# Kernel optimization log

Hardware: AMD Instinct MI355X
Metric: run time of the kernel (lower is better)

## Reference

```python
import math
import jax, jax.numpy as jnp
import numpy as np

MODEL_DIM = 4096
NUM_EXPERTS = 64
NUM_TOKENS = 8192
CAPACITY_FACTOR = 1.0


def setup_inputs() -> dict:
    key = jax.random.key(0)
    kx, kw = jax.random.split(key)
    x = jax.random.normal(kx, (NUM_TOKENS, MODEL_DIM), dtype=jnp.float32)
    # nn.Linear weight: [num_experts, model_dim]
    W = jax.random.normal(kw, (NUM_EXPERTS, MODEL_DIM), dtype=jnp.float32) * (1.0 / math.sqrt(MODEL_DIM))
    return {"x": x, "W": W}


def reference(x, W):
    # gating projection (no bias), cast to fp32 as in top1gating
    logits = jnp.matmul(x, W.T).astype(jnp.float32)  # [S, E]
    num_tokens, num_experts = logits.shape
    capacity = int(CAPACITY_FACTOR * math.ceil(num_tokens / num_experts))

    indices1_s = jnp.argmax(logits, axis=1)                        # [S]
    gates = jax.nn.softmax(logits, axis=1)                         # [S, E]
    mask1 = jax.nn.one_hot(indices1_s, num_experts, dtype=jnp.float32)  # [S, E]
    gates1_s = jnp.sum(gates * mask1, axis=1)                      # [S]
    # per-expert running position of each routed token
    locations1 = jnp.cumsum(mask1, axis=0) - 1.0                   # [S, E]
    locations1_s = jnp.sum(locations1 * mask1, axis=1)             # [S]

    return (indices1_s.astype(jnp.int32),
            capacity,
            locations1_s.astype(jnp.int32),
            gates1_s,
            num_experts)
```

## Files before the change

### kernel.cpp

```cpp
#include <hip/hip_runtime.h>
#include <math.h>

#define NTOK 8192
#define MDIM 4096
#define NEXP 64
#define CAPACITY 128.0f

#define OFF_IDX  0
#define OFF_CAP  8192
#define OFF_LOC  8193
#define OFF_GATE 16385
#define OFF_NE   24577

#define KC 64

#define WS_CNT_OFF  0
#define WS_RK_OFF   8192
#define WS_W_OFF    16384
#define WS_PART_OFF (16384 + (3 * NEXP * MDIM) / 2)

using bf16x8 = __attribute__((ext_vector_type(8))) short;
using f32x4  = __attribute__((ext_vector_type(4))) float;

static __device__ __forceinline__ unsigned short f2bf(float f) {
    union { float f; unsigned u; } v; v.f = f;
    unsigned r = v.u + 0x7fffu + ((v.u >> 16) & 1u);
    return (unsigned short)(r >> 16);
}
static __device__ __forceinline__ float bf2f(unsigned short h) {
    union { unsigned u; float f; } v; v.u = ((unsigned)h) << 16;
    return v.f;
}

__global__ __launch_bounds__(256) void prep_w(
    const float* __restrict__ W, unsigned short* __restrict__ Ws)
{
    const int gid = blockIdx.x * 256 + threadIdx.x;
    const int e   = gid >> 10;
    const int f4  = gid & 1023;
    float4 v = ((const float4*)W)[e * 1024 + f4];
    float av[4] = {v.x, v.y, v.z, v.w};
    unsigned short h[3][4];
    #pragma unroll
    for (int j = 0; j < 4; ++j) {
        float a = av[j];
        unsigned short b1 = f2bf(a);  float r1 = a  - bf2f(b1);
        unsigned short b2 = f2bf(r1); float r2 = r1 - bf2f(b2);
        unsigned short b3 = f2bf(r2);
        h[0][j] = b1; h[1][j] = b2; h[2][j] = b3;
    }
    #pragma unroll
    for (int t = 0; t < 3; ++t)
        *(ushort4*)&Ws[((size_t)(t * 64 + e)) * MDIM + f4 * 4] =
            make_ushort4(h[t][0], h[t][1], h[t][2], h[t][3]);
}

template<int S>
__global__ __launch_bounds__(256, 3) void gate_mfma(
    const float* __restrict__ x,
    const unsigned short* __restrict__ Ws,
    float* __restrict__ part)
{
    constexpr int KSL = MDIM / S;
    constexpr int NCH = KSL / KC;

    __shared__ __align__(16) float4 xs[2][4][16][16];

    const int tid   = threadIdx.x;
    const int lane  = tid & 63;
    const int wv    = tid >> 6;
    const int m     = lane & 15;
    const int g     = lane >> 4;
    const int tok0  = blockIdx.x * 64;
    const int slice = blockIdx.y;
    const int k0    = slice * KSL;

    const float4* __restrict__ x4 = (const float4*)x;
    const unsigned short* __restrict__ wp =
        Ws + (size_t)m * MDIM + k0 + g * 8;

    auto stage = [&](int c, int b) {
        #pragma unroll
        for (int j = 0; j < 4; ++j) {
            const int tl  = j * 4 + (lane >> 4);
            const int src = (lane & 15) ^ (tl & 7);
            const float4* gsrc = x4 + (size_t)(tok0 + wv * 16 + tl) * (MDIM / 4)
                                 + (k0 >> 2) + c * 16 + src;
            void* ldst = (void*)&xs[b][wv][j * 4][0];
            __builtin_amdgcn_global_load_lds(
                (const __attribute__((address_space(1))) void*)gsrc,
                (__attribute__((address_space(3))) void*)ldst, 16, 0, 0);
        }
    };

    auto readx = [&](int b, int ks, float4& lo, float4& hi) {
        const int l0 = ks * 8 + g * 2;
        lo = xs[b][wv][m][(l0    ) ^ (m & 7)];
        hi = xs[b][wv][m][(l0 + 1) ^ (m & 7)];
    };

    auto cvt = [&](float4 lo, float4 hi, bf16x8& r0, bf16x8& r1, bf16x8& r2) {
        float f[8] = {lo.x, lo.y, lo.z, lo.w, hi.x, hi.y, hi.z, hi.w};
        #pragma unroll
        for (int j = 0; j < 8; ++j) {
            float a = f[j];
            unsigned short b1 = f2bf(a);  float t1 = a  - bf2f(b1);
            unsigned short b2 = f2bf(t1); float t2 = t1 - bf2f(b2);
            unsigned short b3 = f2bf(t2);
            r0[j] = (short)b1; r1[j] = (short)b2; r2[j] = (short)b3;
        }
    };

    f32x4 acc[4];
    #pragma unroll
    for (int nt = 0; nt < 4; ++nt) acc[nt] = (f32x4){0.f, 0.f, 0.f, 0.f};

    auto step = [&](const bf16x8* a, bf16x8 w[3][4]) {
        #pragma unroll
        for (int nt = 0; nt < 4; ++nt)
            acc[nt] = __builtin_amdgcn_mfma_f32_16x16x32_bf16(a[2], w[0][nt], acc[nt], 0, 0, 0);
        #pragma unroll
        for (int nt = 0; nt < 4; ++nt)
            acc[nt] = __builtin_amdgcn_mfma_f32_16x16x32_bf16(a[0], w[2][nt], acc[nt], 0, 0, 0);
        #pragma unroll
        for (int nt = 0; nt < 4; ++nt)
            acc[nt] = __builtin_amdgcn_mfma_f32_16x16x32_bf16(a[1], w[1][nt], acc[nt], 0, 0, 0);
        #pragma unroll
        for (int nt = 0; nt < 4; ++nt)
            acc[nt] = __builtin_amdgcn_mfma_f32_16x16x32_bf16(a[1], w[0][nt], acc[nt], 0, 0, 0);
        #pragma unroll
        for (int nt = 0; nt < 4; ++nt)
            acc[nt] = __builtin_amdgcn_mfma_f32_16x16x32_bf16(a[0], w[1][nt], acc[nt], 0, 0, 0);
        #pragma unroll
        for (int nt = 0; nt < 4; ++nt)
            acc[nt] = __builtin_amdgcn_mfma_f32_16x16x32_bf16(a[0], w[0][nt], acc[nt], 0, 0, 0);
    };

    stage(0, 0);

    for (int c = 0; c < NCH; ++c) {
        const int cur = c & 1;
        if (c + 1 < NCH) stage(c + 1, cur ^ 1);

        bf16x8 w0[3][4], w1[3][4];
        const unsigned short* q = wp + c * KC;
        #pragma unroll
        for (int t = 0; t < 3; ++t)
            #pragma unroll
            for (int nt = 0; nt < 4; ++nt)
                w0[t][nt] = *(const bf16x8*)(q + (size_t)(t * 64 + nt * 16) * MDIM);

        float4 lo0, hi0, lo1, hi1;
        readx(cur, 0, lo0, hi0);
        readx(cur, 1, lo1, hi1);
        bf16x8 a0[3], a1[3];
        cvt(lo0, hi0, a0[0], a0[1], a0[2]);
        cvt(lo1, hi1, a1[0], a1[1], a1[2]);

        #pragma unroll
        for (int t = 0; t < 3; ++t)
            #pragma unroll
            for (int nt = 0; nt < 4; ++nt)
                w1[t][nt] = *(const bf16x8*)(q + (size_t)(t * 64 + nt * 16) * MDIM + 32);

        step(a0, w0);
        step(a1, w1);
    }

    #pragma unroll
    for (int nt = 0; nt < 4; ++nt)
        #pragma unroll
        for (int r = 0; r < 4; ++r) {
            const int tokr = tok0 + wv * 16 + g * 4 + r;
            part[((size_t)slice * NTOK + tokr) * 64 + nt * 16 + m] = acc[nt][r];
        }
}

template<int S>
__global__ __launch_bounds__(256) void reduce_count(
    const float* __restrict__ part,
    float* __restrict__ out,
    int* __restrict__ cnt,
    int* __restrict__ rk)
{
    __shared__ int eidx[64];

    const int tid  = threadIdx.x;
    const int lane = tid & 63;
    const int wv   = tid >> 6;
    const int tok0 = blockIdx.x * 64;
    const int trel = wv * 16 + (lane >> 2);
    const int tok  = tok0 + trel;
    const int q    = lane & 3;

    const float4* __restrict__ p4 = (const float4*)part;

    float4 a[4];
    #pragma unroll
    for (int r = 0; r < 4; ++r) a[r] = make_float4(0.f, 0.f, 0.f, 0.f);
    for (int s = 0; s < S; ++s) {
        #pragma unroll
        for (int r = 0; r < 4; ++r) {
            float4 v = p4[((size_t)s * NTOK + tok) * 16 + q * 4 + r];
            a[r].x += v.x; a[r].y += v.y; a[r].z += v.z; a[r].w += v.w;
        }
    }

    float vals[16];
    #pragma unroll
    for (int r = 0; r < 4; ++r) {
        vals[r * 4 + 0] = a[r].x; vals[r * 4 + 1] = a[r].y;
        vals[r * 4 + 2] = a[r].z; vals[r * 4 + 3] = a[r].w;
    }

    float bm = vals[0];
    int   be = q * 16;
    #pragma unroll
    for (int j = 1; j < 16; ++j)
        if (vals[j] > bm) { bm = vals[j]; be = q * 16 + j; }
    #pragma unroll
    for (int off = 1; off <= 2; off <<= 1) {
        float om = __shfl_xor(bm, off, 64);
        int   oe = __shfl_xor(be, off, 64);
        if (om > bm || (om == bm && oe < be)) { bm = om; be = oe; }
    }

    float es = 0.f;
    #pragma unroll
    for (int j = 0; j < 16; ++j) es += expf(vals[j] - bm);
    #pragma unroll
    for (int off = 1; off <= 2; off <<= 1)
        es += __shfl_xor(es, off, 64);

    if (q == 0) {
        out[OFF_IDX  + tok] = (float)be;
        out[OFF_GATE + tok] = 1.0f / es;
        eidx[trel] = be;
    }
    __syncthreads();

    if (tid < 64) {
        const int e = eidx[tid];
        const unsigned long long lt =
            (tid == 0) ? 0ull : ((~0ull) >> (64 - tid));
        unsigned long long mymask = 0;
        int myrk = 0;
        for (int ee = 0; ee < 64; ++ee) {
            unsigned long long mb = __ballot(e == ee);
            if (tid == ee) mymask = mb;
            if (e == ee)   myrk   = (int)__popcll(mb & lt);
        }
        cnt[blockIdx.x * 64 + tid] = (int)__popcll(mymask);
        rk[tok0 + tid] = myrk;
    }
    if (tid == 0 && blockIdx.x == 0) {
        out[OFF_CAP] = CAPACITY;
        out[OFF_NE]  = (float)NEXP;
    }
}

__global__ __launch_bounds__(1024) void scan_final(
    const float* __restrict__ idxf,
    const int* __restrict__ cnt,
    const int* __restrict__ rk,
    float* __restrict__ out)
{
    __shared__ int lcnt[128 * 64];
    __shared__ int wtot[16 * 64];

    const int tid  = threadIdx.x;
    const int lane = tid & 63;
    const int w    = tid >> 6;

    #pragma unroll
    for (int j = 0; j < 8; ++j) lcnt[j * 1024 + tid] = cnt[j * 1024 + tid];
    __syncthreads();

    {
        int sum = 0;
        #pragma unroll
        for (int j = 0; j < 8; ++j) sum += lcnt[(w * 8 + j) * 64 + lane];
        wtot[w * 64 + lane] = sum;
    }
    __syncthreads();

    if (tid < 64) {
        int run = 0;
        #pragma unroll
        for (int w2 = 0; w2 < 16; ++w2) {
            int t = wtot[w2 * 64 + tid];
            wtot[w2 * 64 + tid] = run;
            run += t;
        }
    }
    __syncthreads();

    {
        int run = wtot[w * 64 + lane];
        #pragma unroll
        for (int j = 0; j < 8; ++j) {
            int c = w * 8 + j;
            int v = lcnt[c * 64 + lane];
            lcnt[c * 64 + lane] = run;
            run += v;
        }
    }
    __syncthreads();

    #pragma unroll
    for (int j = 0; j < 8; ++j) {
        int s = j * 1024 + tid;
        int e = (int)idxf[s];
        out[OFF_LOC + s] = (float)(lcnt[(s >> 6) * 64 + e] + rk[s]);
    }
}

extern "C" void kernel_launch(void* const* d_in, const int* in_sizes, int n_in,
                              void* d_out, int out_size, void* d_ws, size_t ws_size,
                              hipStream_t stream)
{
    const float* x = (const float*)d_in[0];
    const float* W = (const float*)d_in[1];
    float* out = (float*)d_out;

    int*   cnt  = (int*)d_ws + WS_CNT_OFF;
    int*   rk   = (int*)d_ws + WS_RK_OFF;
    unsigned short* Ws = (unsigned short*)((int*)d_ws + WS_W_OFF);
    float* part = (float*)d_ws + WS_PART_OFF;

    prep_w<<<256, 256, 0, stream>>>(W, Ws);

    const size_t base = (size_t)WS_PART_OFF * 4;
    const size_t per_slice = (size_t)NTOK * 64 * 4;

    if (ws_size >= base + 8 * per_slice) {
        gate_mfma<8><<<dim3(128, 8), 256, 0, stream>>>(x, Ws, part);
        reduce_count<8><<<128, 256, 0, stream>>>(part, out, cnt, rk);
    } else if (ws_size >= base + 4 * per_slice) {
        gate_mfma<4><<<dim3(128, 4), 256, 0, stream>>>(x, Ws, part);
        reduce_count<4><<<128, 256, 0, stream>>>(part, out, cnt, rk);
    } else if (ws_size >= base + 2 * per_slice) {
        gate_mfma<2><<<dim3(128, 2), 256, 0, stream>>>(x, Ws, part);
        reduce_count<2><<<128, 256, 0, stream>>>(part, out, cnt, rk);
    } else {
        gate_mfma<1><<<dim3(128, 1), 256, 0, stream>>>(x, Ws, part);
        reduce_count<1><<<128, 256, 0, stream>>>(part, out, cnt, rk);
    }

    scan_final<<<1, 1024, 0, stream>>>(out + OFF_IDX, cnt, rk, out);
}
```

Baseline: 273.4 us.

## Retile gating GEMM to single-wave 32-token blocks and parallelize location scan

The gating matmul now uses one-wave blocks covering 32 tokens (two 16-row groups sharing each weight fragment) with a 32-wide K chunk, and splits K into up to 16 slices, so the grid has many more blocks. The reduce kernel is adapted to 32-token blocks. The single-block 1024-thread scan is replaced by a per-expert wave-shuffle scan kernel plus a parallel emit kernel. The aim is better CU occupancy and latency hiding, and removing the serial single-block tail. In exchange there are more partial-sum writes and reads and an extra kernel launch.

```diff
diff --git a/kernel.cpp b/kernel.cpp
--- a/kernel.cpp
+++ b/kernel.cpp
@@ -12,12 +12,15 @@
 #define OFF_GATE 16385
 #define OFF_NE   24577
 
-#define KC 64
+#define KC 32
+
+#define NCHK 256
 
 #define WS_CNT_OFF  0
-#define WS_RK_OFF   8192
-#define WS_W_OFF    16384
-#define WS_PART_OFF (16384 + (3 * NEXP * MDIM) / 2)
+#define WS_RK_OFF   16384
+#define WS_SB_OFF   24576
+#define WS_W_OFF    40960
+#define WS_PART_OFF (40960 + (3 * NEXP * MDIM) / 2)
 
 using bf16x8 = __attribute__((ext_vector_type(8))) short;
 using f32x4  = __attribute__((ext_vector_type(4))) float;
@@ -56,7 +59,7 @@
 }
 
 template<int S>
-__global__ __launch_bounds__(256, 3) void gate_mfma(
+__global__ __launch_bounds__(64, 3) void gate_mfma(
     const float* __restrict__ x,
     const unsigned short* __restrict__ Ws,
     float* __restrict__ part)
@@ -64,14 +67,12 @@
     constexpr int KSL = MDIM / S;
     constexpr int NCH = KSL / KC;
 
-    __shared__ __align__(16) float4 xs[2][4][16][16];
-
-    const int tid   = threadIdx.x;
-    const int lane  = tid & 63;
-    const int wv    = tid >> 6;
+    __shared__ __align__(16) float4 xs[2][32][8];
+
+    const int lane  = threadIdx.x & 63;
     const int m     = lane & 15;
     const int g     = lane >> 4;
-    const int tok0  = blockIdx.x * 64;
+    const int tok0  = blockIdx.x * 32;
     const int slice = blockIdx.y;
     const int k0    = slice * KSL;
 
@@ -82,21 +83,15 @@
     auto stage = [&](int c, int b) {
         #pragma unroll
         for (int j = 0; j < 4; ++j) {
-            const int tl  = j * 4 + (lane >> 4);
-            const int src = (lane & 15) ^ (tl & 7);
-            const float4* gsrc = x4 + (size_t)(tok0 + wv * 16 + tl) * (MDIM / 4)
-                                 + (k0 >> 2) + c * 16 + src;
-            void* ldst = (void*)&xs[b][wv][j * 4][0];
+            const int row  = j * 8 + (lane >> 3);
+            const int srcs = (lane & 7) ^ (row & 7);
+            const float4* gsrc = x4 + (size_t)(tok0 + row) * (MDIM / 4)
+                                 + (k0 >> 2) + c * 8 + srcs;
+            void* ldst = (void*)&xs[b][j * 8][0];
             __builtin_amdgcn_global_load_lds(
                 (const __attribute__((address_space(1))) void*)gsrc,
                 (__attribute__((address_space(3))) void*)ldst, 16, 0, 0);
         }
-    };
-
-    auto readx = [&](int b, int ks, float4& lo, float4& hi) {
-        const int l0 = ks * 8 + g * 2;
-        lo = xs[b][wv][m][(l0    ) ^ (m & 7)];
-        hi = xs[b][wv][m][(l0 + 1) ^ (m & 7)];
     };
 
     auto cvt = [&](float4 lo, float4 hi, bf16x8& r0, bf16x8& r1, bf16x8& r2) {
@@ -111,69 +106,77 @@
         }
     };
 
-    f32x4 acc[4];
-    #pragma unroll
-    for (int nt = 0; nt < 4; ++nt) acc[nt] = (f32x4){0.f, 0.f, 0.f, 0.f};
-
-    auto step = [&](const bf16x8* a, bf16x8 w[3][4]) {
-        #pragma unroll
-        for (int nt = 0; nt < 4; ++nt)
-            acc[nt] = __builtin_amdgcn_mfma_f32_16x16x32_bf16(a[2], w[0][nt], acc[nt], 0, 0, 0);
-        #pragma unroll
-        for (int nt = 0; nt < 4; ++nt)
-            acc[nt] = __builtin_amdgcn_mfma_f32_16x16x32_bf16(a[0], w[2][nt], acc[nt], 0, 0, 0);
-        #pragma unroll
-        for (int nt = 0; nt < 4; ++nt)
-            acc[nt] = __builtin_amdgcn_mfma_f32_16x16x32_bf16(a[1], w[1][nt], acc[nt], 0, 0, 0);
-        #pragma unroll
-        for (int nt = 0; nt < 4; ++nt)
-            acc[nt] = __builtin_amdgcn_mfma_f32_16x16x32_bf16(a[1], w[0][nt], acc[nt], 0, 0, 0);
-        #pragma unroll
-        for (int nt = 0; nt < 4; ++nt)
-            acc[nt] = __builtin_amdgcn_mfma_f32_16x16x32_bf16(a[0], w[1][nt], acc[nt], 0, 0, 0);
-        #pragma unroll
-        for (int nt = 0; nt < 4; ++nt)
-            acc[nt] = __builtin_amdgcn_mfma_f32_16x16x32_bf16(a[0], w[0][nt], acc[nt], 0, 0, 0);
-    };
+    f32x4 acc[2][4];
+    #pragma unroll
+    for (int gr = 0; gr < 2; ++gr)
+        #pragma unroll
+        for (int nt = 0; nt < 4; ++nt) acc[gr][nt] = (f32x4){0.f, 0.f, 0.f, 0.f};
 
     stage(0, 0);
 
     for (int c = 0; c < NCH; ++c) {
         const int cur = c & 1;
+
+        bf16x8 w[3][4];
+        const unsigned short* q = wp + c * KC;
+        #pragma unroll
+        for (int t = 0; t < 3; ++t)
+            #pragma unroll
+            for (int nt = 0; nt < 4; ++nt)
+                w[t][nt] = *(const bf16x8*)(q + (size_t)(t * 64 + nt * 16) * MDIM);
+
         if (c + 1 < NCH) stage(c + 1, cur ^ 1);
 
-        bf16x8 w0[3][4], w1[3][4];
-        const unsigned short* q = wp + c * KC;
-        #pragma unroll
-        for (int t = 0; t < 3; ++t)
-            #pragma unroll
-            for (int nt = 0; nt < 4; ++nt)
-                w0[t][nt] = *(const bf16x8*)(q + (size_t)(t * 64 + nt * 16) * MDIM);
-
-        float4 lo0, hi0, lo1, hi1;
-        readx(cur, 0, lo0, hi0);
-        readx(cur, 1, lo1, hi1);
-        bf16x8 a0[3], a1[3];
-        cvt(lo0, hi0, a0[0], a0[1], a0[2]);
-        cvt(lo1, hi1, a1[0], a1[1], a1[2]);
-
-        #pragma unroll
-        for (int t = 0; t < 3; ++t)
-            #pragma unroll
-            for (int nt = 0; nt < 4; ++nt)
-                w1[t][nt] = *(const bf16x8*)(q + (size_t)(t * 64 + nt * 16) * MDIM + 32);
-
-        step(a0, w0);
-        step(a1, w1);
-    }
-
-    #pragma unroll
-    for (int nt = 0; nt < 4; ++nt)
-        #pragma unroll
-        for (int r = 0; r < 4; ++r) {
-            const int tokr = tok0 + wv * 16 + g * 4 + r;
-            part[((size_t)slice * NTOK + tokr) * 64 + nt * 16 + m] = acc[nt][r];
-        }
+        bf16x8 a[2][3];
+        #pragma unroll
+        for (int gr = 0; gr < 2; ++gr) {
+            const int row = gr * 16 + m;
+            float4 lo = xs[cur][row][(2 * g    ) ^ (m & 7)];
+            float4 hi = xs[cur][row][(2 * g + 1) ^ (m & 7)];
+            cvt(lo, hi, a[gr][0], a[gr][1], a[gr][2]);
+        }
+
+        #pragma unroll
+        for (int gr = 0; gr < 2; ++gr)
+            #pragma unroll
+            for (int nt = 0; nt < 4; ++nt)
+                acc[gr][nt] = __builtin_amdgcn_mfma_f32_16x16x32_bf16(a[gr][2], w[0][nt], acc[gr][nt], 0, 0, 0);
+        #pragma unroll
+        for (int gr = 0; gr < 2; ++gr)
+            #pragma unroll
+            for (int nt = 0; nt < 4; ++nt)
+                acc[gr][nt] = __builtin_amdgcn_mfma_f32_16x16x32_bf16(a[gr][0], w[2][nt], acc[gr][nt], 0, 0, 0);
+        #pragma unroll
+        for (int gr = 0; gr < 2; ++gr)
+            #pragma unroll
+            for (int nt = 0; nt < 4; ++nt)
+                acc[gr][nt] = __builtin_amdgcn_mfma_f32_16x16x32_bf16(a[gr][1], w[1][nt], acc[gr][nt], 0, 0, 0);
+        #pragma unroll
+        for (int gr = 0; gr < 2; ++gr)
+            #pragma unroll
+            for (int nt = 0; nt < 4; ++nt)
+                acc[gr][nt] = __builtin_amdgcn_mfma_f32_16x16x32_bf16(a[gr][1], w[0][nt], acc[gr][nt], 0, 0, 0);
+        #pragma unroll
+        for (int gr = 0; gr < 2; ++gr)
+            #pragma unroll
+            for (int nt = 0; nt < 4; ++nt)
+                acc[gr][nt] = __builtin_amdgcn_mfma_f32_16x16x32_bf16(a[gr][0], w[1][nt], acc[gr][nt], 0, 0, 0);
+        #pragma unroll
+        for (int gr = 0; gr < 2; ++gr)
+            #pragma unroll
+            for (int nt = 0; nt < 4; ++nt)
+                acc[gr][nt] = __builtin_amdgcn_mfma_f32_16x16x32_bf16(a[gr][0], w[0][nt], acc[gr][nt], 0, 0, 0);
+    }
+
+    #pragma unroll
+    for (int gr = 0; gr < 2; ++gr)
+        #pragma unroll
+        for (int nt = 0; nt < 4; ++nt)
+            #pragma unroll
+            for (int r = 0; r < 4; ++r) {
+                const int tokr = tok0 + gr * 16 + g * 4 + r;
+                part[((size_t)slice * NTOK + tokr) * 64 + nt * 16 + m] = acc[gr][nt][r];
+            }
 }
 
 template<int S>
@@ -183,43 +186,37 @@
     int* __restrict__ cnt,
     int* __restrict__ rk)
 {
-    __shared__ int eidx[64];
+    __shared__ int eidx[32];
 
     const int tid  = threadIdx.x;
-    const int lane = tid & 63;
-    const int wv   = tid >> 6;
-    const int tok0 = blockIdx.x * 64;
-    const int trel = wv * 16 + (lane >> 2);
+    const int tok0 = blockIdx.x * 32;
+    const int trel = tid >> 3;
     const int tok  = tok0 + trel;
-    const int q    = lane & 3;
+    const int q    = tid & 7;
 
     const float4* __restrict__ p4 = (const float4*)part;
 
-    float4 a[4];
-    #pragma unroll
-    for (int r = 0; r < 4; ++r) a[r] = make_float4(0.f, 0.f, 0.f, 0.f);
+    float4 a[2];
+    #pragma unroll
+    for (int r = 0; r < 2; ++r) a[r] = make_float4(0.f, 0.f, 0.f, 0.f);
     for (int s = 0; s < S; ++s) {
         #pragma unroll
-        for (int r = 0; r < 4; ++r) {
-            float4 v = p4[((size_t)s * NTOK + tok) * 16 + q * 4 + r];
+        for (int r = 0; r < 2; ++r) {
+            float4 v = p4[((size_t)s * NTOK + tok) * 16 + q * 2 + r];
             a[r].x += v.x; a[r].y += v.y; a[r].z += v.z; a[r].w += v.w;
         }
     }
 
-    float vals[16];
-    #pragma unroll
-    for (int r = 0; r < 4; ++r) {
-        vals[r * 4 + 0] = a[r].x; vals[r * 4 + 1] = a[r].y;
-        vals[r * 4 + 2] = a[r].z; vals[r * 4 + 3] = a[r].w;
-    }
+    float vals[8] = {a[0].x, a[0].y, a[0].z, a[0].w,
+                     a[1].x, a[1].y, a[1].z, a[1].w};
 
     float bm = vals[0];
-    int   be = q * 16;
-    #pragma unroll
-    for (int j = 1; j < 16; ++j)
-        if (vals[j] > bm) { bm = vals[j]; be = q * 16 + j; }
-    #pragma unroll
-    for (int off = 1; off <= 2; off <<= 1) {
+    int   be = q * 8;
+    #pragma unroll
+    for (int j = 1; j < 8; ++j)
+        if (vals[j] > bm) { bm = vals[j]; be = q * 8 + j; }
+    #pragma unroll
+    for (int off = 1; off <= 4; off <<= 1) {
         float om = __shfl_xor(bm, off, 64);
         int   oe = __shfl_xor(be, off, 64);
         if (om > bm || (om == bm && oe < be)) { bm = om; be = oe; }
@@ -227,9 +224,9 @@
 
     float es = 0.f;
     #pragma unroll
-    for (int j = 0; j < 16; ++j) es += expf(vals[j] - bm);
-    #pragma unroll
-    for (int off = 1; off <= 2; off <<= 1)
+    for (int j = 0; j < 8; ++j) es += expf(vals[j] - bm);
+    #pragma unroll
+    for (int off = 1; off <= 4; off <<= 1)
         es += __shfl_xor(es, off, 64);
 
     if (q == 0) {
@@ -240,7 +237,7 @@
     __syncthreads();
 
     if (tid < 64) {
-        const int e = eidx[tid];
+        const int e = (tid < 32) ? eidx[tid] : -1;
         const unsigned long long lt =
             (tid == 0) ? 0ull : ((~0ull) >> (64 - tid));
         unsigned long long mymask = 0;
@@ -251,7 +248,7 @@
             if (e == ee)   myrk   = (int)__popcll(mb & lt);
         }
         cnt[blockIdx.x * 64 + tid] = (int)__popcll(mymask);
-        rk[tok0 + tid] = myrk;
+        if (tid < 32) rk[tok0 + tid] = myrk;
     }
     if (tid == 0 && blockIdx.x == 0) {
         out[OFF_CAP] = CAPACITY;
@@ -259,60 +256,46 @@
     }
 }
 
-__global__ __launch_bounds__(1024) void scan_final(
+__global__ __launch_bounds__(64) void scan_e(
+    const int* __restrict__ cnt, int* __restrict__ sb)
+{
+    const int e = blockIdx.x;
+    const int l = threadIdx.x & 63;
+
+    int v[4], s[4];
+    #pragma unroll
+    for (int seg = 0; seg < 4; ++seg)
+        v[seg] = cnt[(seg * 64 + l) * 64 + e];
+
+    #pragma unroll
+    for (int seg = 0; seg < 4; ++seg) {
+        int sv = v[seg];
+        #pragma unroll
+        for (int off = 1; off <= 32; off <<= 1) {
+            int u = __shfl_up(sv, off, 64);
+            if (l >= off) sv += u;
+        }
+        s[seg] = sv;
+    }
+    int t0 = __shfl(s[0], 63, 64);
+    int t1 = __shfl(s[1], 63, 64);
+    int t2 = __shfl(s[2], 63, 64);
+    s[1] += t0; s[2] += t0 + t1; s[3] += t0 + t1 + t2;
+
+    #pragma unroll
+    for (int seg = 0; seg < 4; ++seg)
+        sb[(seg * 64 + l) * 64 + e] = s[seg] - v[seg];
+}
+
+__global__ __launch_bounds__(256) void emit_loc(
     const float* __restrict__ idxf,
-    const int* __restrict__ cnt,
+    const int* __restrict__ sb,
     const int* __restrict__ rk,
     float* __restrict__ out)
 {
-    __shared__ int lcnt[128 * 64];
-    __shared__ int wtot[16 * 64];
-
-    const int tid  = threadIdx.x;
-    const int lane = tid & 63;
-    const int w    = tid >> 6;
-
-    #pragma unroll
-    for (int j = 0; j < 8; ++j) lcnt[j * 1024 + tid] = cnt[j * 1024 + tid];
-    __syncthreads();
-
-    {
-        int sum = 0;
-        #pragma unroll
-        for (int j = 0; j < 8; ++j) sum += lcnt[(w * 8 + j) * 64 + lane];
-        wtot[w * 64 + lane] = sum;
-    }
-    __syncthreads();
-
-    if (tid < 64) {
-        int run = 0;
-        #pragma unroll
-        for (int w2 = 0; w2 < 16; ++w2) {
-            int t = wtot[w2 * 64 + tid];
-            wtot[w2 * 64 + tid] = run;
-            run += t;
-        }
-    }
-    __syncthreads();
-
-    {
-        int run = wtot[w * 64 + lane];
-        #pragma unroll
-        for (int j = 0; j < 8; ++j) {
-            int c = w * 8 + j;
-            int v = lcnt[c * 64 + lane];
-            lcnt[c * 64 + lane] = run;
-            run += v;
-        }
-    }
-    __syncthreads();
-
-    #pragma unroll
-    for (int j = 0; j < 8; ++j) {
-        int s = j * 1024 + tid;
-        int e = (int)idxf[s];
-        out[OFF_LOC + s] = (float)(lcnt[(s >> 6) * 64 + e] + rk[s]);
-    }
+    const int s = blockIdx.x * 256 + threadIdx.x;
+    const int e = (int)idxf[s];
+    out[OFF_LOC + s] = (float)(sb[(s >> 5) * 64 + e] + rk[s]);
 }
 
 extern "C" void kernel_launch(void* const* d_in, const int* in_sizes, int n_in,
@@ -325,6 +308,7 @@
 
     int*   cnt  = (int*)d_ws + WS_CNT_OFF;
     int*   rk   = (int*)d_ws + WS_RK_OFF;
+    int*   sb   = (int*)d_ws + WS_SB_OFF;
     unsigned short* Ws = (unsigned short*)((int*)d_ws + WS_W_OFF);
     float* part = (float*)d_ws + WS_PART_OFF;
 
@@ -333,19 +317,23 @@
     const size_t base = (size_t)WS_PART_OFF * 4;
     const size_t per_slice = (size_t)NTOK * 64 * 4;
 
-    if (ws_size >= base + 8 * per_slice) {
-        gate_mfma<8><<<dim3(128, 8), 256, 0, stream>>>(x, Ws, part);
-        reduce_count<8><<<128, 256, 0, stream>>>(part, out, cnt, rk);
+    if (ws_size >= base + 16 * per_slice) {
+        gate_mfma<16><<<dim3(256, 16), 64, 0, stream>>>(x, Ws, part);
+        reduce_count<16><<<256, 256, 0, stream>>>(part, out, cnt, rk);
+    } else if (ws_size >= base + 8 * per_slice) {
+        gate_mfma<8><<<dim3(256, 8), 64, 0, stream>>>(x, Ws, part);
+        reduce_count<8><<<256, 256, 0, stream>>>(part, out, cnt, rk);
     } else if (ws_size >= base + 4 * per_slice) {
-        gate_mfma<4><<<dim3(128, 4), 256, 0, stream>>>(x, Ws, part);
-        reduce_count<4><<<128, 256, 0, stream>>>(part, out, cnt, rk);
+        gate_mfma<4><<<dim3(256, 4), 64, 0, stream>>>(x, Ws, part);
+        reduce_count<4><<<256, 256, 0, stream>>>(part, out, cnt, rk);
     } else if (ws_size >= base + 2 * per_slice) {
-        gate_mfma<2><<<dim3(128, 2), 256, 0, stream>>>(x, Ws, part);
-        reduce_count<2><<<128, 256, 0, stream>>>(part, out, cnt, rk);
+        gate_mfma<2><<<dim3(256, 2), 64, 0, stream>>>(x, Ws, part);
+        reduce_count<2><<<256, 256, 0, stream>>>(part, out, cnt, rk);
     } else {
-        gate_mfma<1><<<dim3(128, 1), 256, 0, stream>>>(x, Ws, part);
-        reduce_count<1><<<128, 256, 0, stream>>>(part, out, cnt, rk);
-    }
-
-    scan_final<<<1, 1024, 0, stream>>>(out + OFF_IDX, cnt, rk, out);
-}
+        gate_mfma<1><<<dim3(256, 1), 64, 0, stream>>>(x, Ws, part);
+        reduce_count<1><<<256, 256, 0, stream>>>(part, out, cnt, rk);
+    }
+
+    scan_e<<<64, 64, 0, stream>>>(cnt, sb);
+    emit_loc<<<32, 256, 0, stream>>>(out + OFF_IDX, sb, rk, out);
+}
```

Result: faster. 260.1 us (-4.9%).
